# Kernel tuning notes

Measured on AMD Instinct MI355X. Metric: run time of the kernel, lower is better.

The kernel has to match this reference:

```python
import jax, jax.numpy as jnp
import numpy as np

T, B, I = 1000, 16, 440   # time, batch, input feat
H, P = 1024, 512          # cell size, projection size


def setup_inputs() -> dict:
    key = jax.random.key(0)
    ks = jax.random.split(key, 14)
    s_in = 1.0 / np.sqrt(I)
    s_p = 1.0 / np.sqrt(P)
    s_h = 1.0 / np.sqrt(H)
    inp = {
        "x": jax.random.normal(ks[0], (T, B, I), jnp.float32),
        # input->gate linears (bias=True since no batchnorm/laynorm)
        "wfx_w": jax.random.uniform(ks[1], (H, I), jnp.float32, -s_in, s_in),
        "wfx_b": jax.random.uniform(ks[2], (H,), jnp.float32, -s_in, s_in),
        "wix_w": jax.random.uniform(ks[3], (H, I), jnp.float32, -s_in, s_in),
        "wix_b": jax.random.uniform(ks[4], (H,), jnp.float32, -s_in, s_in),
        "wox_w": jax.random.uniform(ks[5], (H, I), jnp.float32, -s_in, s_in),
        "wox_b": jax.random.uniform(ks[6], (H,), jnp.float32, -s_in, s_in),
        "wcx_w": jax.random.uniform(ks[7], (H, I), jnp.float32, -s_in, s_in),
        "wcx_b": jax.random.uniform(ks[8], (H,), jnp.float32, -s_in, s_in),
        # recurrent projections (bias=False)
        "tfy_w": jax.random.uniform(ks[9], (H, P), jnp.float32, -s_p, s_p),
        "tiy_w": jax.random.uniform(ks[10], (H, P), jnp.float32, -s_p, s_p),
        "toy_w": jax.random.uniform(ks[11], (H, P), jnp.float32, -s_p, s_p),
        "tcy_w": jax.random.uniform(ks[12], (H, P), jnp.float32, -s_p, s_p),
        # output projection h -> y (bias=False)
        "wym_w": jax.random.uniform(ks[13], (P, H), jnp.float32, -s_h, s_h),
    }
    return inp


def reference(x, wfx_w, wfx_b, wix_w, wix_b, wox_w, wox_b, wcx_w, wcx_b,
              tfy_w, tiy_w, toy_w, tcy_w, wym_w):
    # Precompute input-to-gate projections for all timesteps: [T,B,H]
    gf = jnp.einsum('tbi,hi->tbh', x, wfx_w) + wfx_b
    gi = jnp.einsum('tbi,hi->tbh', x, wix_w) + wix_b
    go = jnp.einsum('tbi,hi->tbh', x, wox_w) + wox_b
    gc = jnp.einsum('tbi,hi->tbh', x, wcx_w) + wcx_b

    b = x.shape[1]
    c0 = jnp.zeros((b, H), x.dtype)  # h_init in source (used as cell state)
    y0 = jnp.zeros((b, P), x.dtype)
    drop_mask = jnp.asarray(1.0, x.dtype)  # test mode: 1 - drop, drop=0.0

    def step(carry, g):
        ct, yt = carry
        gf_t, gi_t, go_t, gc_t = g
        it = jax.nn.sigmoid(gi_t + yt @ tiy_w.T)
        ft = jax.nn.sigmoid(gf_t + yt @ tfy_w.T)
        ot = jax.nn.sigmoid(go_t + yt @ toy_w.T)
        ct = it * jnp.tanh(gc_t + yt @ tcy_w.T) * drop_mask + ft * ct
        ht = ot * jnp.tanh(ct)
        yt = ht @ wym_w.T
        return (ct, yt), ht

    _, h = jax.lax.scan(step, (c0, y0), (gf, gi, go, gc))
    return h  # [T, B, H]
```

## Files before the change

kernel.cpp:

```cpp
#include <hip/hip_runtime.h>
#include <hip/hip_fp16.h>
#include <stdint.h>

#define T_STEPS 1000
#define BATCH   16
#define IFEAT   440
#define KPAD    448
#define HDIM    1024
#define PDIM    512
#define NWG     64

typedef _Float16 f16x8 __attribute__((ext_vector_type(8)));
typedef _Float16 f16x4 __attribute__((ext_vector_type(4)));
typedef float    f32x4 __attribute__((ext_vector_type(4)));
typedef uint32_t u32x4 __attribute__((ext_vector_type(4)));

union F16x8U { f16x8 v; u32x4 w; };

#define OFF_HB    0u
#define OFF_XH    65536u
#define OFF_W4    (OFF_XH + 14336000u)
#define OFF_TG    (OFF_W4 + 3670016u)
#define OFF_WYT   (OFF_TG + 4194304u)
#define OFF_M     (OFF_WYT + 1048576u)
#define OFF_GX    (OFF_M + 8388608u)

__device__ __forceinline__ float sigm_(float x)  { return 1.f / (1.f + __expf(-x)); }
__device__ __forceinline__ float tanh_(float x)  { return 1.f - 2.f / (1.f + __expf(2.f * x)); }

__global__ void init_hb(unsigned short* __restrict__ HB) {
    int i = blockIdx.x * 256 + threadIdx.x;
    HB[i] = (i < BATCH * HDIM) ? (unsigned short)0x0000 : (unsigned short)0x0001;
}

__global__ void prep_x(const float* __restrict__ x, _Float16* __restrict__ xh) {
    int idx = blockIdx.x * 256 + threadIdx.x;
    const int total = T_STEPS * BATCH * KPAD;
    for (; idx < total; idx += gridDim.x * 256) {
        int k = idx % KPAD;
        int row = idx / KPAD;
        float v = (k < IFEAT) ? x[row * IFEAT + k] : 0.f;
        xh[idx] = (_Float16)v;
    }
}

__global__ void prep_w(const float* __restrict__ wi, const float* __restrict__ wf,
                       const float* __restrict__ wo, const float* __restrict__ wc,
                       const float* __restrict__ ti, const float* __restrict__ tf,
                       const float* __restrict__ to_, const float* __restrict__ tc,
                       const float* __restrict__ wym,
                       _Float16* __restrict__ W4, _Float16* __restrict__ TG,
                       _Float16* __restrict__ WYT) {
    int tid = blockIdx.x * 256 + threadIdx.x;
    int stride = gridDim.x * 256;
    const float* const Wsrc[4] = {wi, wf, wo, wc};
    const float* const Tsrc[4] = {ti, tf, to_, tc};
    const int totW = 4 * HDIM * KPAD;
    for (int idx = tid; idx < totW; idx += stride) {
        int k = idx % KPAD; int gh = idx / KPAD;
        int h = gh % HDIM;  int g = gh / HDIM;
        W4[idx] = (_Float16)((k < IFEAT) ? Wsrc[g][h * IFEAT + k] : 0.f);
    }
    const int totT = 4 * HDIM * PDIM;
    for (int idx = tid; idx < totT; idx += stride) {
        int p = idx % PDIM; int gh = idx / PDIM;
        int h = gh % HDIM;  int g = gh / HDIM;
        TG[idx] = (_Float16)Tsrc[g][h * PDIM + p];
    }
    const int totY = HDIM * PDIM;
    for (int idx = tid; idx < totY; idx += stride) {
        int p = idx % PDIM; int hh = idx / PDIM;
        WYT[idx] = (_Float16)wym[p * HDIM + hh];
    }
}

__global__ __launch_bounds__(256) void mgemm(const _Float16* __restrict__ TG,
                                             const _Float16* __restrict__ WYT,
                                             _Float16* __restrict__ M) {
    int wave = threadIdx.x >> 6, l = threadIdx.x & 63;
    int lo = l & 15, quad = l >> 4;
    int tile = blockIdx.x * 4 + wave;
    int g = tile >> 12;
    int ht = (tile >> 6) & 63;
    int hht = tile & 63;
    const _Float16* Ar = TG  + ((size_t)(g * HDIM + ht * 16 + lo)) * PDIM;
    const _Float16* Br = WYT + ((size_t)(hht * 16 + lo)) * PDIM;
    f32x4 acc = {0.f, 0.f, 0.f, 0.f};
#pragma unroll
    for (int cc = 0; cc < 16; ++cc) {
        f16x8 a = *(const f16x8*)(Ar + cc * 32 + quad * 8);
        f16x8 b = *(const f16x8*)(Br + cc * 32 + quad * 8);
        acc = __builtin_amdgcn_mfma_f32_16x16x32_f16(a, b, acc, 0, 0, 0);
    }
    _Float16* dst = M + (size_t)g * HDIM * HDIM;
#pragma unroll
    for (int r = 0; r < 4; ++r)
        dst[(size_t)(ht * 16 + quad * 4 + r) * HDIM + hht * 16 + lo] = (_Float16)acc[r];
}

#define TT 4
__global__ __launch_bounds__(256) void phase1(const _Float16* __restrict__ xh,
                                              const _Float16* __restrict__ W4,
                                              const float* __restrict__ bI,
                                              const float* __restrict__ bF,
                                              const float* __restrict__ bO,
                                              const float* __restrict__ bC,
                                              _Float16* __restrict__ GX) {
    __shared__ _Float16 sx[TT * 16 * 456];
    const int t0 = blockIdx.x * TT;
    for (int c = threadIdx.x; c < TT * 16 * 56; c += 256) {
        int kc = c % 56, rowi = c / 56;
        *(f16x8*)(sx + rowi * 456 + kc * 8) =
            *(const f16x8*)(xh + ((size_t)(t0 * 16 + rowi)) * KPAD + kc * 8);
    }
    __syncthreads();
    const int wave = threadIdx.x >> 6, l = threadIdx.x & 63;
    const int lo = l & 15, quad = l >> 4;
    const int g = wave;
    const float* bias = (g == 0) ? bI : (g == 1) ? bF : (g == 2) ? bO : bC;
    for (int htp = 0; htp < 32; ++htp) {
        const int ht0 = htp * 2, ht1 = htp * 2 + 1;
        f16x8 A0[14], A1[14];
        const _Float16* Ar0 = W4 + ((size_t)(g * HDIM + ht0 * 16 + lo)) * KPAD;
        const _Float16* Ar1 = Ar0 + (size_t)16 * KPAD;
#pragma unroll
        for (int cc = 0; cc < 14; ++cc) {
            A0[cc] = *(const f16x8*)(Ar0 + cc * 32 + quad * 8);
            A1[cc] = *(const f16x8*)(Ar1 + cc * 32 + quad * 8);
        }
        float b0[4], b1[4];
#pragma unroll
        for (int r = 0; r < 4; ++r) {
            b0[r] = bias[ht0 * 16 + quad * 4 + r];
            b1[r] = bias[ht1 * 16 + quad * 4 + r];
        }
        for (int t = 0; t < TT; ++t) {
            f32x4 acc0 = {0.f, 0.f, 0.f, 0.f}, acc1 = {0.f, 0.f, 0.f, 0.f};
#pragma unroll
            for (int cc = 0; cc < 14; ++cc) {
                f16x8 b = *(const f16x8*)(sx + (t * 16 + lo) * 456 + cc * 32 + quad * 8);
                acc0 = __builtin_amdgcn_mfma_f32_16x16x32_f16(A0[cc], b, acc0, 0, 0, 0);
                acc1 = __builtin_amdgcn_mfma_f32_16x16x32_f16(A1[cc], b, acc1, 0, 0, 0);
            }
            size_t tbase = ((size_t)(t0 + t) * 4 + g) * 64;
            f16x4 h0, h1;
#pragma unroll
            for (int r = 0; r < 4; ++r) {
                h0[r] = (_Float16)(acc0[r] + b0[r]);
                h1[r] = (_Float16)(acc1[r] + b1[r]);
            }
            *(f16x4*)(GX + ((tbase + ht0) * 64 + l) * 4) = h0;
            *(f16x4*)(GX + ((tbase + ht1) * 64 + l) * 4) = h1;
        }
    }
}

__global__ __launch_bounds__(256, 1) void recur(const _Float16* __restrict__ GX,
                                                const _Float16* __restrict__ Mw,
                                                _Float16* __restrict__ HB,
                                                float* __restrict__ out) {
    const int tid = threadIdx.x, wave = tid >> 6, l = tid & 63;
    const int lo = l & 15, quad = l >> 4;
    const int ht = blockIdx.x;
    const int kbase = wave * 256;

    f16x8 A[4][8];
#pragma unroll
    for (int g = 0; g < 4; ++g) {
        const _Float16* Ar = Mw + ((size_t)g * HDIM + ht * 16 + lo) * HDIM + kbase;
#pragma unroll
        for (int cc = 0; cc < 8; ++cc)
            A[g][cc] = *(const f16x8*)(Ar + cc * 32 + quad * 8);
    }

    __shared__ float P[2][4][4][64][4];
    f32x4 ct = {0.f, 0.f, 0.f, 0.f};

    f16x4 gxbuf[2][4];
    if (wave < 2) {
#pragma unroll
        for (int g = 0; g < 4; ++g) {
            gxbuf[0][g] = *(const f16x4*)(GX + ((((size_t)0 * 4 + g) * 64 + ht) * 64 + l) * 4);
            gxbuf[1][g] = *(const f16x4*)(GX + ((((size_t)1 * 4 + g) * 64 + ht) * 64 + l) * 4);
        }
    }

    const _Float16* hb0 = HB + (size_t)lo * HDIM + kbase + quad * 8;
    _Float16* hs0 = HB + (size_t)lo * HDIM + ht * 16 + quad * 4;

    auto step = [&](int t, int slot) {
        const int par = t & 1;
        const uint32_t expw = ((t >> 1) & 1) ? 0x00010001u : 0u;
        const uint64_t pollA = (uint64_t)(uintptr_t)(hb0 + (size_t)par * BATCH * HDIM);

        F16x8U B[8];
        while (true) {
            asm volatile(
                "global_load_dwordx4 %0, %8, off sc1\n\t"
                "global_load_dwordx4 %1, %8, off offset:64 sc1\n\t"
                "global_load_dwordx4 %2, %8, off offset:128 sc1\n\t"
                "global_load_dwordx4 %3, %8, off offset:192 sc1\n\t"
                "global_load_dwordx4 %4, %8, off offset:256 sc1\n\t"
                "global_load_dwordx4 %5, %8, off offset:320 sc1\n\t"
                "global_load_dwordx4 %6, %8, off offset:384 sc1\n\t"
                "global_load_dwordx4 %7, %8, off offset:448 sc1\n\t"
                "s_waitcnt vmcnt(0)"
                : "=&v"(B[0].w), "=&v"(B[1].w), "=&v"(B[2].w), "=&v"(B[3].w),
                  "=&v"(B[4].w), "=&v"(B[5].w), "=&v"(B[6].w), "=&v"(B[7].w)
                : "v"(pollA)
                : "memory");
            uint32_t bad = 0;
#pragma unroll
            for (int c = 0; c < 8; ++c)
#pragma unroll
                for (int j = 0; j < 4; ++j)
                    bad |= (B[c].w[j] ^ expw) & 0x00010001u;
            if (__all(bad == 0)) break;
        }

        f32x4 acc[4];
#pragma unroll
        for (int g = 0; g < 4; ++g) acc[g] = (f32x4){0.f, 0.f, 0.f, 0.f};
#pragma unroll
        for (int cc = 0; cc < 8; ++cc) {
#pragma unroll
            for (int g = 0; g < 4; ++g)
                acc[g] = __builtin_amdgcn_mfma_f32_16x16x32_f16(A[g][cc], B[cc].v, acc[g], 0, 0, 0);
        }
#pragma unroll
        for (int g = 0; g < 4; ++g)
            *(f32x4*)&P[par][wave][g][l][0] = acc[g];
        __syncthreads();

        if (wave < 2) {
            int tp = (t + 2 < T_STEPS) ? (t + 2) : (T_STEPS - 1);
            f16x4 npf[4];
#pragma unroll
            for (int g = 0; g < 4; ++g)
                npf[g] = *(const f16x4*)(GX + ((((size_t)tp * 4 + g) * 64 + ht) * 64 + l) * 4);

            f32x4 pre[4];
#pragma unroll
            for (int g = 0; g < 4; ++g) {
                f32x4 s = *(const f32x4*)&P[par][0][g][l][0];
#pragma unroll
                for (int k = 1; k < 4; ++k) s = s + *(const f32x4*)&P[par][k][g][l][0];
                f16x4 gv = gxbuf[slot][g];
#pragma unroll
                for (int r = 0; r < 4; ++r) s[r] += (float)gv[r];
                pre[g] = s;
            }
            f32x4 hv; f16x4 hh;
#pragma unroll
            for (int r = 0; r < 4; ++r) {
                float it = sigm_(pre[0][r]);
                float ft = sigm_(pre[1][r]);
                float ot = sigm_(pre[2][r]);
                float gt = tanh_(pre[3][r]);
                ct[r] = it * gt + ft * ct[r];
                float h = ot * tanh_(ct[r]);
                hv[r] = h; hh[r] = (_Float16)h;
            }
            if (wave == 0) {
                unsigned long long bits; __builtin_memcpy(&bits, &hh, 8);
                const unsigned long long TAG = 0x0001000100010001ULL;
                unsigned long long genw = (unsigned long long)(((t + 1) >> 1) & 1);
                bits = (bits & ~TAG) | (genw * TAG);
                uint64_t sA = (uint64_t)(uintptr_t)(hs0 + (size_t)((t + 1) & 1) * BATCH * HDIM);
                asm volatile("global_store_dwordx2 %0, %1, off sc1"
                             :: "v"(sA), "v"(bits) : "memory");
            } else {
                __builtin_nontemporal_store(hv,
                    (f32x4*)(out + ((size_t)t * BATCH + lo) * HDIM + ht * 16 + quad * 4));
            }
#pragma unroll
            for (int g = 0; g < 4; ++g) gxbuf[slot][g] = npf[g];
        }
    };

    for (int t = 0; t < T_STEPS; t += 2) {
        step(t, 0);
        step(t + 1, 1);
    }
}

extern "C" void kernel_launch(void* const* d_in, const int* in_sizes, int n_in,
                              void* d_out, int out_size, void* d_ws, size_t ws_size,
                              hipStream_t stream) {
    const float* x    = (const float*)d_in[0];
    const float* wfxw = (const float*)d_in[1];
    const float* wfxb = (const float*)d_in[2];
    const float* wixw = (const float*)d_in[3];
    const float* wixb = (const float*)d_in[4];
    const float* woxw = (const float*)d_in[5];
    const float* woxb = (const float*)d_in[6];
    const float* wcxw = (const float*)d_in[7];
    const float* wcxb = (const float*)d_in[8];
    const float* tfyw = (const float*)d_in[9];
    const float* tiyw = (const float*)d_in[10];
    const float* toyw = (const float*)d_in[11];
    const float* tcyw = (const float*)d_in[12];
    const float* wymw = (const float*)d_in[13];

    char* ws = (char*)d_ws;
    _Float16*  HB    = (_Float16*)(ws + OFF_HB);
    _Float16*  XH    = (_Float16*)(ws + OFF_XH);
    _Float16*  W4    = (_Float16*)(ws + OFF_W4);
    _Float16*  TG    = (_Float16*)(ws + OFF_TG);
    _Float16*  WYT   = (_Float16*)(ws + OFF_WYT);
    _Float16*  Mw    = (_Float16*)(ws + OFF_M);
    _Float16*  GX    = (_Float16*)(ws + OFF_GX);
    float* out = (float*)d_out;

    init_hb<<<128, 256, 0, stream>>>((unsigned short*)HB);
    prep_x<<<4096, 256, 0, stream>>>(x, XH);
    prep_w<<<2048, 256, 0, stream>>>(wixw, wfxw, woxw, wcxw,
                                     tiyw, tfyw, toyw, tcyw, wymw,
                                     W4, TG, WYT);
    mgemm<<<4096, 256, 0, stream>>>(TG, WYT, Mw);
    phase1<<<250, 256, 0, stream>>>(XH, W4, wixb, wfxb, woxb, wcxb, GX);
    recur<<<NWG, 256, 0, stream>>>(GX, Mw, HB, out);
}
```

Before: 4.810 ms.

## Specialize waves: four MFMA producer waves and a dedicated gate-update consumer wave

Splits the recurrent kernel into four producer waves that poll for the previous hidden state and compute the recurrent matmul, and a fifth consumer wave that reduces partial sums, applies gate nonlinearities and publishes h. Producers and consumer hand off through double-buffered shared memory with raw barriers, replacing the full-block syncthreads. The poll check is also simplified to OR/AND reductions of tag bits. The consumer now issues both the hidden-state and output stores alone, which may lengthen the critical path.

```diff
diff --git a/kernel.cpp b/kernel.cpp
--- a/kernel.cpp
+++ b/kernel.cpp
@@ -155,84 +155,90 @@
     }
 }
 
-__global__ __launch_bounds__(256, 1) void recur(const _Float16* __restrict__ GX,
+__global__ __launch_bounds__(320, 1) void recur(const _Float16* __restrict__ GX,
                                                 const _Float16* __restrict__ Mw,
                                                 _Float16* __restrict__ HB,
                                                 float* __restrict__ out) {
     const int tid = threadIdx.x, wave = tid >> 6, l = tid & 63;
     const int lo = l & 15, quad = l >> 4;
     const int ht = blockIdx.x;
-    const int kbase = wave * 256;
-
-    f16x8 A[4][8];
-#pragma unroll
-    for (int g = 0; g < 4; ++g) {
-        const _Float16* Ar = Mw + ((size_t)g * HDIM + ht * 16 + lo) * HDIM + kbase;
-#pragma unroll
-        for (int cc = 0; cc < 8; ++cc)
-            A[g][cc] = *(const f16x8*)(Ar + cc * 32 + quad * 8);
-    }
 
     __shared__ float P[2][4][4][64][4];
-    f32x4 ct = {0.f, 0.f, 0.f, 0.f};
-
-    f16x4 gxbuf[2][4];
-    if (wave < 2) {
+
+    if (wave < 4) {
+        const int kbase = wave * 256;
+        f16x8 A[4][8];
+#pragma unroll
+        for (int g = 0; g < 4; ++g) {
+            const _Float16* Ar = Mw + ((size_t)g * HDIM + ht * 16 + lo) * HDIM + kbase;
+#pragma unroll
+            for (int cc = 0; cc < 8; ++cc)
+                A[g][cc] = *(const f16x8*)(Ar + cc * 32 + quad * 8);
+        }
+        const _Float16* hb0 = HB + (size_t)lo * HDIM + kbase + quad * 8;
+
+        for (int t = 0; t < T_STEPS; ++t) {
+            const int par = t & 1;
+            const int gen = (t >> 1) & 1;
+            const uint64_t pollA = (uint64_t)(uintptr_t)(hb0 + (size_t)par * BATCH * HDIM);
+
+            F16x8U B[8];
+            while (true) {
+                asm volatile(
+                    "global_load_dwordx4 %0, %8, off sc1\n\t"
+                    "global_load_dwordx4 %1, %8, off offset:64 sc1\n\t"
+                    "global_load_dwordx4 %2, %8, off offset:128 sc1\n\t"
+                    "global_load_dwordx4 %3, %8, off offset:192 sc1\n\t"
+                    "global_load_dwordx4 %4, %8, off offset:256 sc1\n\t"
+                    "global_load_dwordx4 %5, %8, off offset:320 sc1\n\t"
+                    "global_load_dwordx4 %6, %8, off offset:384 sc1\n\t"
+                    "global_load_dwordx4 %7, %8, off offset:448 sc1\n\t"
+                    "s_waitcnt vmcnt(0)"
+                    : "=&v"(B[0].w), "=&v"(B[1].w), "=&v"(B[2].w), "=&v"(B[3].w),
+                      "=&v"(B[4].w), "=&v"(B[5].w), "=&v"(B[6].w), "=&v"(B[7].w)
+                    : "v"(pollA)
+                    : "memory");
+                if (gen == 0) {
+                    u32x4 r = B[0].w | B[1].w | B[2].w | B[3].w |
+                              B[4].w | B[5].w | B[6].w | B[7].w;
+                    uint32_t b = (r[0] | r[1] | r[2] | r[3]) & 1u;
+                    if (__all(b == 0u)) break;
+                } else {
+                    u32x4 r = B[0].w & B[1].w & B[2].w & B[3].w &
+                              B[4].w & B[5].w & B[6].w & B[7].w;
+                    uint32_t b = (r[0] & r[1] & r[2] & r[3]) & 1u;
+                    if (__all(b == 1u)) break;
+                }
+            }
+
+            f32x4 acc[4];
+#pragma unroll
+            for (int g = 0; g < 4; ++g) acc[g] = (f32x4){0.f, 0.f, 0.f, 0.f};
+#pragma unroll
+            for (int cc = 0; cc < 8; ++cc) {
+#pragma unroll
+                for (int g = 0; g < 4; ++g)
+                    acc[g] = __builtin_amdgcn_mfma_f32_16x16x32_f16(A[g][cc], B[cc].v, acc[g], 0, 0, 0);
+            }
+#pragma unroll
+            for (int g = 0; g < 4; ++g)
+                *(f32x4*)&P[par][wave][g][l][0] = acc[g];
+            asm volatile("s_waitcnt lgkmcnt(0)\n\ts_barrier" ::: "memory");
+        }
+    } else {
+        f32x4 ct = {0.f, 0.f, 0.f, 0.f};
+        f16x4 gxbuf[2][4];
 #pragma unroll
         for (int g = 0; g < 4; ++g) {
             gxbuf[0][g] = *(const f16x4*)(GX + ((((size_t)0 * 4 + g) * 64 + ht) * 64 + l) * 4);
             gxbuf[1][g] = *(const f16x4*)(GX + ((((size_t)1 * 4 + g) * 64 + ht) * 64 + l) * 4);
         }
-    }
-
-    const _Float16* hb0 = HB + (size_t)lo * HDIM + kbase + quad * 8;
-    _Float16* hs0 = HB + (size_t)lo * HDIM + ht * 16 + quad * 4;
-
-    auto step = [&](int t, int slot) {
-        const int par = t & 1;
-        const uint32_t expw = ((t >> 1) & 1) ? 0x00010001u : 0u;
-        const uint64_t pollA = (uint64_t)(uintptr_t)(hb0 + (size_t)par * BATCH * HDIM);
-
-        F16x8U B[8];
-        while (true) {
-            asm volatile(
-                "global_load_dwordx4 %0, %8, off sc1\n\t"
-                "global_load_dwordx4 %1, %8, off offset:64 sc1\n\t"
-                "global_load_dwordx4 %2, %8, off offset:128 sc1\n\t"
-                "global_load_dwordx4 %3, %8, off offset:192 sc1\n\t"
-                "global_load_dwordx4 %4, %8, off offset:256 sc1\n\t"
-                "global_load_dwordx4 %5, %8, off offset:320 sc1\n\t"
-                "global_load_dwordx4 %6, %8, off offset:384 sc1\n\t"
-                "global_load_dwordx4 %7, %8, off offset:448 sc1\n\t"
-                "s_waitcnt vmcnt(0)"
-                : "=&v"(B[0].w), "=&v"(B[1].w), "=&v"(B[2].w), "=&v"(B[3].w),
-                  "=&v"(B[4].w), "=&v"(B[5].w), "=&v"(B[6].w), "=&v"(B[7].w)
-                : "v"(pollA)
-                : "memory");
-            uint32_t bad = 0;
-#pragma unroll
-            for (int c = 0; c < 8; ++c)
-#pragma unroll
-                for (int j = 0; j < 4; ++j)
-                    bad |= (B[c].w[j] ^ expw) & 0x00010001u;
-            if (__all(bad == 0)) break;
-        }
-
-        f32x4 acc[4];
-#pragma unroll
-        for (int g = 0; g < 4; ++g) acc[g] = (f32x4){0.f, 0.f, 0.f, 0.f};
-#pragma unroll
-        for (int cc = 0; cc < 8; ++cc) {
-#pragma unroll
-            for (int g = 0; g < 4; ++g)
-                acc[g] = __builtin_amdgcn_mfma_f32_16x16x32_f16(A[g][cc], B[cc].v, acc[g], 0, 0, 0);
-        }
-#pragma unroll
-        for (int g = 0; g < 4; ++g)
-            *(f32x4*)&P[par][wave][g][l][0] = acc[g];
-        __syncthreads();
-
-        if (wave < 2) {
+        _Float16* hs0 = HB + (size_t)lo * HDIM + ht * 16 + quad * 4;
+
+        for (int t = 0; t < T_STEPS; ++t) {
+            const int par = t & 1;
+            asm volatile("s_barrier" ::: "memory");
+
             int tp = (t + 2 < T_STEPS) ? (t + 2) : (T_STEPS - 1);
             f16x4 npf[4];
 #pragma unroll
@@ -245,7 +251,7 @@
                 f32x4 s = *(const f32x4*)&P[par][0][g][l][0];
 #pragma unroll
                 for (int k = 1; k < 4; ++k) s = s + *(const f32x4*)&P[par][k][g][l][0];
-                f16x4 gv = gxbuf[slot][g];
+                f16x4 gv = gxbuf[par][g];
 #pragma unroll
                 for (int r = 0; r < 4; ++r) s[r] += (float)gv[r];
                 pre[g] = s;
@@ -261,26 +267,18 @@
                 float h = ot * tanh_(ct[r]);
                 hv[r] = h; hh[r] = (_Float16)h;
             }
-            if (wave == 0) {
-                unsigned long long bits; __builtin_memcpy(&bits, &hh, 8);
-                const unsigned long long TAG = 0x0001000100010001ULL;
-                unsigned long long genw = (unsigned long long)(((t + 1) >> 1) & 1);
-                bits = (bits & ~TAG) | (genw * TAG);
-                uint64_t sA = (uint64_t)(uintptr_t)(hs0 + (size_t)((t + 1) & 1) * BATCH * HDIM);
-                asm volatile("global_store_dwordx2 %0, %1, off sc1"
-                             :: "v"(sA), "v"(bits) : "memory");
-            } else {
-                __builtin_nontemporal_store(hv,
-                    (f32x4*)(out + ((size_t)t * BATCH + lo) * HDIM + ht * 16 + quad * 4));
-            }
-#pragma unroll
-            for (int g = 0; g < 4; ++g) gxbuf[slot][g] = npf[g];
-        }
-    };
-
-    for (int t = 0; t < T_STEPS; t += 2) {
-        step(t, 0);
-        step(t + 1, 1);
+            unsigned long long bits; __builtin_memcpy(&bits, &hh, 8);
+            const unsigned long long TAG = 0x0001000100010001ULL;
+            unsigned long long genw = (unsigned long long)(((t + 1) >> 1) & 1);
+            bits = (bits & ~TAG) | (genw * TAG);
+            uint64_t sA = (uint64_t)(uintptr_t)(hs0 + (size_t)((t + 1) & 1) * BATCH * HDIM);
+            asm volatile("global_store_dwordx2 %0, %1, off sc1"
+                         :: "v"(sA), "v"(bits) : "memory");
+            __builtin_nontemporal_store(hv,
+                (f32x4*)(out + ((size_t)t * BATCH + lo) * HDIM + ht * 16 + quad * 4));
+#pragma unroll
+            for (int g = 0; g < 4; ++g) gxbuf[par][g] = npf[g];
+        }
     }
 }
 
@@ -319,5 +317,5 @@
                                      W4, TG, WYT);
     mgemm<<<4096, 256, 0, stream>>>(TG, WYT, Mw);
     phase1<<<250, 256, 0, stream>>>(XH, W4, wixb, wfxb, woxb, wcxb, GX);
-    recur<<<NWG, 256, 0, stream>>>(GX, Mw, HB, out);
-}
+    recur<<<NWG, 320, 0, stream>>>(GX, Mw, HB, out);
+}
```

After: 8.844 ms. +83.9%, slower.
